# Optimization experiments

Measured on AMD Instinct MI355X. Metric: run time of the kernel, lower is better.

## Reference

```python
import jax, jax.numpy as jnp
import numpy as np

B, T = 128, 256
H = 200                      # hidden_dim
EMB, POSD, NERD = 300, 30, 30
VOCAB, NPOS, NNER = 40000, 50, 25
NCLASS = 2
IN = EMB + POSD + NERD


def setup_inputs():
    key = jax.random.key(0)
    ks = jax.random.split(key, 32)
    words = jax.random.randint(ks[0], (B, T), 1, VOCAB)
    lengths = jax.random.randint(ks[1], (B,), T // 2, T + 1)
    t = jnp.arange(T)
    masks = (t[None, :] >= lengths[:, None]).astype(jnp.int64)  # 1 = pad
    pos = jax.random.randint(ks[2], (B, T), 0, NPOS)
    ner = jax.random.randint(ks[3], (B, T), 0, NNER)

    def span_pos(k, span):  # relative position encoding, 0 on entity span
        start = jax.random.randint(k, (B,), 0, T // 2 - span)
        rel = t[None, :] - start[:, None]
        return jnp.where(rel < 0, rel, jnp.where(rel < span, 0, rel - span + 1)).astype(jnp.int64)

    subj_pos = span_pos(ks[4], 3)
    obj_pos = span_pos(ks[5], 2)

    s = 0.08
    def rn(k, shape):
        return jax.random.normal(k, shape, dtype=jnp.float32) * s

    p = {}
    p["emb_w"] = rn(ks[6], (VOCAB, EMB)).at[0].set(0.0)  # PAD row
    p["pos_w"] = rn(ks[7], (NPOS, POSD))
    p["ner_w"] = rn(ks[8], (NNER, NERD))
    dims = [IN, 2 * H]
    i = 9
    for l in range(2):
        for d in ("f", "b"):
            p["w_ih_l%d%s" % (l, d)] = rn(ks[i], (4 * H, dims[l])); i += 1
            p["w_hh_l%d%s" % (l, d)] = rn(ks[i], (4 * H, H)); i += 1
            p["b_l%d%s" % (l, d)] = rn(ks[i], (4 * H,)); i += 1
    p["wo_w"] = rn(ks[i], (H, 2 * H)); p["wo_b"] = rn(ks[i + 1], (H,))
    p["ws_w"] = rn(ks[i + 2], (H, 2 * H)); p["ws_b"] = rn(ks[i + 3], (H,))
    p["wg_w"] = rn(ks[i + 4], (H, 2 * H)); p["wg_b"] = rn(ks[i + 5], (H,))
    p["cls_w"] = rn(ks[i + 6], (NCLASS, H)); p["cls_b"] = rn(ks[i + 7], (NCLASS,))
    return dict(words=words, masks=masks, pos=pos, ner=ner,
                subj_pos=subj_pos, obj_pos=obj_pos, **p)


def lstm_dir(x, keep, w_ih, w_hh, b, reverse):
    """Packed-sequence-equivalent LSTM: state frozen and output zeroed at pads.
    x: [B,T,D], keep: [B,T] (1.0 = real token). Returns ([B,T,H], final h [B,H])."""
    Hh = w_hh.shape[1]

    def step(carry, inp):
        h, c = carry
        xt, mt = inp  # [B,D], [B,1]
        g = xt @ w_ih.T + h @ w_hh.T + b
        i, f, gg, o = jnp.split(g, 4, axis=-1)  # torch gate order i,f,g,o
        cn = jax.nn.sigmoid(f) * c + jax.nn.sigmoid(i) * jnp.tanh(gg)
        hn = jax.nn.sigmoid(o) * jnp.tanh(cn)
        h = mt * hn + (1.0 - mt) * h
        c = mt * cn + (1.0 - mt) * c
        return (h, c), h * mt

    b_ = x.shape[0]
    h0 = jnp.zeros((b_, Hh), x.dtype)
    xs = (jnp.swapaxes(x, 0, 1), keep.T[..., None])
    (hT, _), ys = jax.lax.scan(step, (h0, h0), xs, reverse=reverse)
    return jnp.swapaxes(ys, 0, 1), hT


def attn_pool(q, kv, pad):
    # single-query attention: q [B,D], kv [B,T,D], pad [B,T] bool
    d_k = q.shape[-1]
    scores = jnp.einsum("bd,btd->bt", q, kv) / jnp.sqrt(jnp.float32(d_k))
    scores = jnp.where(pad, jnp.float32(-1e9), scores)
    p = jax.nn.softmax(scores, axis=-1)
    return jnp.einsum("bt,btd->bd", p, kv)


def _forward(words, masks, pos, ner, subj_pos, obj_pos,
             emb_w, pos_w, ner_w,
             w_ih_l0f, w_hh_l0f, b_l0f, w_ih_l0b, w_hh_l0b, b_l0b,
             w_ih_l1f, w_hh_l1f, b_l1f, w_ih_l1b, w_hh_l1b, b_l1b,
             wo_w, wo_b, ws_w, ws_b, wg_w, wg_b, cls_w, cls_b):
    embs = jnp.concatenate([emb_w[words], pos_w[pos], ner_w[ner]], axis=-1)
    keep = (masks == 0).astype(embs.dtype)
    of0, _ = lstm_dir(embs, keep, w_ih_l0f, w_hh_l0f, b_l0f, False)
    ob0, _ = lstm_dir(embs, keep, w_ih_l0b, w_hh_l0b, b_l0b, True)
    x1 = jnp.concatenate([of0, ob0], axis=-1)
    of1, hf1 = lstm_dir(x1, keep, w_ih_l1f, w_hh_l1f, b_l1f, False)
    ob1, hb1 = lstm_dir(x1, keep, w_ih_l1b, w_hh_l1b, b_l1b, True)
    rnn_out = jnp.concatenate([of1, ob1], axis=-1)  # [B,T,2H]

    pad = masks != 0
    # masked gather-sum over entity spans: (rel_pos + mask) == 0 selects span tokens
    subj_sel = ((subj_pos + masks) == 0).astype(rnn_out.dtype)[..., None]
    obj_sel = ((obj_pos + masks) == 0).astype(rnn_out.dtype)[..., None]
    subj_h = jnp.sum(rnn_out * subj_sel, axis=1)  # [B,2H]
    obj_h = jnp.sum(rnn_out * obj_sel, axis=1)
    glob_h = jnp.concatenate([hb1, hf1], axis=-1)  # hidden[-1]=last bwd, hidden[-2]=last fwd

    obj_a = attn_pool(obj_h, rnn_out, pad)
    subj_a = attn_pool(subj_h, rnn_out, pad)
    glob_a = attn_pool(glob_h, rnn_out, pad)

    h = jax.nn.relu(obj_a @ wo_w.T + wo_b + subj_a @ ws_w.T + ws_b + glob_a @ wg_w.T + wg_b)
    return h @ cls_w.T + cls_b  # [B, NCLASS]


def reference(words, masks, pos, ner, subj_pos, obj_pos,
              emb_w, pos_w, ner_w,
              w_ih_l0f, w_hh_l0f, b_l0f, w_ih_l0b, w_hh_l0b, b_l0b,
              w_ih_l1f, w_hh_l1f, b_l1f, w_ih_l1b, w_hh_l1b, b_l1b,
              wo_w, wo_b, ws_w, ws_b, wg_w, wg_b, cls_w, cls_b):
    return _forward(words, masks, pos, ner, subj_pos, obj_pos,
                    emb_w, pos_w, ner_w,
                    w_ih_l0f, w_hh_l0f, b_l0f, w_ih_l0b, w_hh_l0b, b_l0b,
                    w_ih_l1f, w_hh_l1f, b_l1f, w_ih_l1b, w_hh_l1b, b_l1b,
                    wo_w, wo_b, ws_w, ws_b, wg_w, wg_b, cls_w, cls_b)
```

## Files before the change

kernel.cpp:

```cpp
#include <hip/hip_runtime.h>
#include <hip/hip_bf16.h>
#include <math.h>

constexpr int B = 128;
constexpr int T = 256;
constexpr int H = 200;
constexpr int G4 = 800;
constexpr int BT = B * T;
constexpr int K0 = 360, K0P = 384;
constexpr int K1 = 400, K1P = 416;

typedef __bf16 bf16x8 __attribute__((ext_vector_type(8)));
typedef float f32x4 __attribute__((ext_vector_type(4)));
typedef _Float16 half2v __attribute__((ext_vector_type(2)));
typedef unsigned uix4 __attribute__((ext_vector_type(4)));

__device__ __forceinline__ float bfr2f(unsigned short u) {
  union { unsigned int i; float f; } x;
  x.i = ((unsigned int)u) << 16;
  return x.f;
}
__device__ __forceinline__ unsigned short f2hu(float f) {
  _Float16 h = (_Float16)f;
  return *(unsigned short*)&h;
}
__device__ __forceinline__ half2v ash2(unsigned u) {
  union { unsigned v; half2v h; } x;
  x.v = u;
  return x.h;
}
__device__ __forceinline__ float sigm(float x) {
  return 1.0f / (1.0f + __expf(-x));
}
__device__ __forceinline__ float tanh_f(float x) {
  float e = __expf(2.0f * x);
  return (e - 1.0f) / (e + 1.0f);
}
__device__ __forceinline__ float ldraw(const void* p, size_t i, int f) {
  return f ? ((const float*)p)[i] : bfr2f(((const unsigned short*)p)[i]);
}

__global__ void detect_dtype(const unsigned short* __restrict__ raw,
                             int* __restrict__ flag) {
  __shared__ int cnt[256];
  int c = 0;
  for (int j = 0; j < 32; ++j) {
    unsigned short u = raw[1024 + threadIdx.x * 32 + j];
    int e = (u >> 7) & 0xFF;
    if (e >= 0xC0) ++c;
  }
  cnt[threadIdx.x] = c;
  __syncthreads();
  for (int off = 128; off > 0; off >>= 1) {
    if (threadIdx.x < off) cnt[threadIdx.x] += cnt[threadIdx.x + off];
    __syncthreads();
  }
  if (threadIdx.x == 0) *flag = (cnt[0] > 16) ? 1 : 0;
}

__global__ void fill_zero(uix4* __restrict__ p, size_t n4) {
  size_t i = (size_t)blockIdx.x * blockDim.x + threadIdx.x;
  size_t stride = (size_t)gridDim.x * blockDim.x;
  uix4 z = {0u, 0u, 0u, 0u};
  for (; i < n4; i += stride) p[i] = z;
}

__global__ void embed_kernel(const int* __restrict__ words,
                             const int* __restrict__ pos,
                             const int* __restrict__ ner,
                             const void* __restrict__ emb_w,
                             const void* __restrict__ pos_w,
                             const void* __restrict__ ner_w,
                             __hip_bfloat16* __restrict__ X0,
                             const int* __restrict__ flag) {
  int bt = blockIdx.x;
  int f = *flag;
  int w = words[bt], p = pos[bt], nr = ner[bt];
  for (int j = threadIdx.x; j < K0P; j += blockDim.x) {
    float v;
    if (j < 300)       v = ldraw(emb_w, (size_t)w * 300 + j, f);
    else if (j < 330)  v = ldraw(pos_w, (size_t)p * 30 + (j - 300), f);
    else if (j < 360)  v = ldraw(ner_w, (size_t)nr * 30 + (j - 330), f);
    else               v = 0.0f;
    X0[(size_t)bt * K0P + j] = __float2bfloat16(v);
  }
}

__global__ void pad_copy2(const void* __restrict__ srcf,
                          const void* __restrict__ srcb,
                          __hip_bfloat16* __restrict__ dst, int K, int Kp,
                          const int* __restrict__ flag) {
  int r = blockIdx.x;
  int f = *flag;
  const void* src = (r < G4) ? srcf : srcb;
  int rr = (r < G4) ? r : r - G4;
  for (int j = threadIdx.x; j < Kp; j += blockDim.x) {
    float v = (j < K) ? ldraw(src, (size_t)rr * K + j, f) : 0.0f;
    dst[(size_t)r * Kp + j] = __float2bfloat16(v);
  }
}

__global__ void pack_whh4(const void* __restrict__ s0, const void* __restrict__ s1,
                          const void* __restrict__ s2, const void* __restrict__ s3,
                          unsigned* __restrict__ dst,
                          const int* __restrict__ flag) {
  int idx = blockIdx.x * blockDim.x + threadIdx.x;
  if (idx >= 4 * G4 * 100) return;
  int f = *flag;
  int m = idx / (G4 * 100);
  int loc = idx - m * (G4 * 100);
  const void* src = (m == 0) ? s0 : (m == 1) ? s1 : (m == 2) ? s2 : s3;
  int n = loc / 100, p = loc - n * 100;
  float lo_f = ldraw(src, (size_t)n * 200 + 2 * p, f);
  float hi_f = ldraw(src, (size_t)n * 200 + 2 * p + 1, f);
  dst[idx] = (unsigned)f2hu(lo_f) | ((unsigned)f2hu(hi_f) << 16);
}

__global__ __launch_bounds__(256) void gemm_bt(
    const __hip_bfloat16* __restrict__ A,
    const __hip_bfloat16* __restrict__ Bm,
    __hip_bfloat16* __restrict__ C,
    int N, int Kp) {
  const int lane = threadIdx.x & 63;
  const int wave = threadIdx.x >> 6;
  const int l15 = lane & 15, quad = lane >> 4;
  const int m0 = blockIdx.x * 64 + (wave & 1) * 32;
  const int n0 = blockIdx.y * 128 + (wave >> 1) * 64;

  f32x4 acc[2][4] = {};

  size_t br[4];
  #pragma unroll
  for (int j = 0; j < 4; ++j) {
    int c = n0 + 16 * j + l15;
    if (c > N - 1) c = N - 1;
    br[j] = (size_t)c * Kp;
  }
  const size_t ar0 = (size_t)(m0 + l15) * Kp;
  const size_t ar1 = (size_t)(m0 + 16 + l15) * Kp;

  for (int k0 = 0; k0 < Kp; k0 += 32) {
    int ko = k0 + quad * 8;
    bf16x8 a0 = *(const bf16x8*)(A + ar0 + ko);
    bf16x8 a1 = *(const bf16x8*)(A + ar1 + ko);
    #pragma unroll
    for (int j = 0; j < 4; ++j) {
      bf16x8 b = *(const bf16x8*)(Bm + br[j] + ko);
      acc[0][j] = __builtin_amdgcn_mfma_f32_16x16x32_bf16(a0, b, acc[0][j], 0, 0, 0);
      acc[1][j] = __builtin_amdgcn_mfma_f32_16x16x32_bf16(a1, b, acc[1][j], 0, 0, 0);
    }
  }
  #pragma unroll
  for (int mi = 0; mi < 2; ++mi)
    #pragma unroll
    for (int ni = 0; ni < 4; ++ni)
      #pragma unroll
      for (int r = 0; r < 4; ++r) {
        int row = m0 + mi * 16 + quad * 4 + r;
        int col = n0 + ni * 16 + l15;
        if (col < N)
          C[(size_t)row * N + col] = __float2bfloat16(acc[mi][ni][r]);
      }
}

__global__ __launch_bounds__(512, 2) void lstm_row(
    const __hip_bfloat16* __restrict__ Gpre,
    const unsigned* __restrict__ Wpack,
    const void* __restrict__ bias_f_raw,
    const void* __restrict__ bias_b_raw,
    const int* __restrict__ masks,
    __hip_bfloat16* __restrict__ out,
    int ostride,
    float* __restrict__ final_h,
    const int* __restrict__ flag)
{
  const int tid = threadIdx.x;
  const int dir = blockIdx.x >> 7;
  const int row = blockIdx.x & 127;
  const int wave = tid >> 6;
  const int lane = tid & 63;
  const int kq = wave & 3;
  const int gs = ((wave >> 2) << 6) | lane;
  const bool tail = (gs >= 96);

  __shared__ __align__(16) _Float16 hsh[256];
  __shared__ float parts[4 * 804];
  __shared__ int lensh[256];
  __shared__ int bigbuf[21504];

  const unsigned* wb = Wpack + (size_t)dir * G4 * 100;

  for (int i = tid; i < 3200; i += 512) {
    int g = i / 100, c = i - g * 100;
    bigbuf[g * 101 + c] = (int)wb[(768 + g) * 100 + c];
  }
  if (tid < 256) lensh[tid] = (masks[row * T + tid] == 0) ? 1 : 0;

  unsigned w[6][25];
  {
    const unsigned* s = wb + gs * 100 + kq * 25;
    #pragma unroll
    for (int j = 0; j < 6; ++j)
      #pragma unroll
      for (int p = 0; p < 25; ++p)
        w[j][p] = s[12800 * j + p];
  }
  const unsigned* wt = (const unsigned*)&bigbuf[(gs - 96) * 101 + kq * 25];

  const int u = tid;
  const int f = *flag;
  const void* braw = dir ? bias_b_raw : bias_f_raw;
  float bI = 0.f, bF = 0.f, bG = 0.f, bO = 0.f;
  if (u < 200) {
    bI = ldraw(braw, u, f);
    bF = ldraw(braw, 200 + u, f);
    bG = ldraw(braw, 400 + u, f);
    bO = ldraw(braw, 600 + u, f);
  }

  if (tid < 256) hsh[tid] = (_Float16)0.0f;
  float creg = 0.0f, hreg = 0.0f;
  __syncthreads();

  for (int off = 128; off > 0; off >>= 1) {
    if (tid < off) lensh[tid] += lensh[tid + off];
    __syncthreads();
  }
  const int len = lensh[0];

  const unsigned short* gp = (const unsigned short*)Gpre + dir * 800;
  const size_t gbase = (size_t)row * T;
  const uix4* hvp = (const uix4*)((const char*)hsh + kq * 128);
  const int hwrite = (u / 50) * 64 + (u % 50);

  #pragma unroll 1
  for (int tt = 0; tt < len; ++tt) {
    const int t = dir ? (len - 1 - tt) : tt;
    const size_t goff = (gbase + t) * 1600;
    unsigned short qI = 0, qF = 0, qG = 0, qO = 0;
    if (u < 200) {
      qI = gp[goff + u];
      qF = gp[goff + 200 + u];
      qG = gp[goff + 400 + u];
      qO = gp[goff + 600 + u];
    }

    uix4 hb[7];
    #pragma unroll
    for (int i = 0; i < 7; ++i) hb[i] = hvp[i];

    float a0 = 0.f, a1 = 0.f, a2 = 0.f, a3 = 0.f, a4 = 0.f, a5 = 0.f;
    #pragma unroll
    for (int p = 0; p < 25; ++p) {
      half2v h2 = ash2(hb[p >> 2][p & 3]);
      a0 = __builtin_amdgcn_fdot2(ash2(w[0][p]), h2, a0, false);
      a1 = __builtin_amdgcn_fdot2(ash2(w[1][p]), h2, a1, false);
      a2 = __builtin_amdgcn_fdot2(ash2(w[2][p]), h2, a2, false);
      a3 = __builtin_amdgcn_fdot2(ash2(w[3][p]), h2, a3, false);
      a4 = __builtin_amdgcn_fdot2(ash2(w[4][p]), h2, a4, false);
      a5 = __builtin_amdgcn_fdot2(ash2(w[5][p]), h2, a5, false);
    }
    const int pb = kq * 804;
    parts[pb + gs]        = a0;
    parts[pb + 128 + gs]  = a1;
    parts[pb + 256 + gs]  = a2;
    parts[pb + 384 + gs]  = a3;
    parts[pb + 512 + gs]  = a4;
    parts[pb + 640 + gs]  = a5;
    if (tail) {
      float a6 = 0.f;
      #pragma unroll
      for (int p = 0; p < 25; ++p)
        a6 = __builtin_amdgcn_fdot2(ash2(wt[p]), ash2(hb[p >> 2][p & 3]), a6, false);
      parts[pb + 672 + gs] = a6;
    }
    __syncthreads();

    if (u < 200) {
      float gi = parts[u]       + parts[804 + u]       + parts[1608 + u]       + parts[2412 + u]       + bI + bfr2f(qI);
      float gf = parts[200 + u] + parts[804 + 200 + u] + parts[1608 + 200 + u] + parts[2412 + 200 + u] + bF + bfr2f(qF);
      float gg = parts[400 + u] + parts[804 + 400 + u] + parts[1608 + 400 + u] + parts[2412 + 400 + u] + bG + bfr2f(qG);
      float go = parts[600 + u] + parts[804 + 600 + u] + parts[1608 + 600 + u] + parts[2412 + 600 + u] + bO + bfr2f(qO);
      float si = sigm(gi), sf = sigm(gf), so = sigm(go);
      float cn = sf * creg + si * tanh_f(gg);
      float hn = so * tanh_f(cn);
      creg = cn;
      hreg = hn;
      hsh[hwrite] = (_Float16)hn;
      out[((size_t)row * T + t) * ostride + dir * H + u] = __float2bfloat16(hn);
    }
    __syncthreads();
  }

  if (final_h != nullptr && u < 200) {
    int col = dir ? u : (H + u);
    final_h[(size_t)row * 400 + col] = hreg;
  }
}

__global__ __launch_bounds__(256) void span_sum(
    const __hip_bfloat16* __restrict__ rnn,
    const int* __restrict__ masks,
    const int* __restrict__ subj_pos,
    const int* __restrict__ obj_pos,
    float* __restrict__ obj_h,
    float* __restrict__ subj_h)
{
  int b = blockIdx.x;
  int tc = threadIdx.x >> 6;
  int dv = threadIdx.x & 63;
  __shared__ float aS[4][400];
  __shared__ float aO[4][400];

  float ss[8] = {}, so[8] = {};
  if (dv < 50) {
    for (int t = tc * 64; t < tc * 64 + 64; ++t) {
      int m = masks[b * T + t];
      int fs = (subj_pos[b * T + t] + m) == 0;
      int fo = (obj_pos[b * T + t] + m) == 0;
      if (fs | fo) {
        uix4 v = *(const uix4*)(rnn + ((size_t)b * T + t) * 400 + dv * 8);
        #pragma unroll
        for (int j = 0; j < 4; ++j) {
          float lo = bfr2f((unsigned short)(v[j] & 0xFFFF));
          float hi = bfr2f((unsigned short)(v[j] >> 16));
          if (fs) { ss[2 * j] += lo; ss[2 * j + 1] += hi; }
          if (fo) { so[2 * j] += lo; so[2 * j + 1] += hi; }
        }
      }
    }
    #pragma unroll
    for (int k = 0; k < 8; ++k) {
      aS[tc][dv * 8 + k] = ss[k];
      aO[tc][dv * 8 + k] = so[k];
    }
  }
  __syncthreads();
  for (int d = threadIdx.x; d < 400; d += 256) {
    subj_h[(size_t)b * 400 + d] = aS[0][d] + aS[1][d] + aS[2][d] + aS[3][d];
    obj_h[(size_t)b * 400 + d]  = aO[0][d] + aO[1][d] + aO[2][d] + aO[3][d];
  }
}

__global__ __launch_bounds__(256) void attn_pool_k(
    const float* __restrict__ qbuf,
    const __hip_bfloat16* __restrict__ rnn,
    const int* __restrict__ masks,
    float* __restrict__ outp)
{
  int b = blockIdx.x & 127;
  int qi = blockIdx.x >> 7;
  __shared__ float qs[400];
  __shared__ float ps[256];
  __shared__ float red[256];
  __shared__ float acc4[4][400];
  const float* q = qbuf + ((size_t)qi * B + b) * 400;
  for (int d = threadIdx.x; d < 400; d += 256) qs[d] = q[d];
  __syncthreads();

  int t = threadIdx.x;
  const uix4* kvv = (const uix4*)(rnn + ((size_t)b * T + t) * 400);
  float s = 0.f;
  #pragma unroll 5
  for (int i = 0; i < 50; ++i) {
    uix4 v = kvv[i];
    #pragma unroll
    for (int j = 0; j < 4; ++j) {
      s += bfr2f((unsigned short)(v[j] & 0xFFFF)) * qs[8 * i + 2 * j];
      s += bfr2f((unsigned short)(v[j] >> 16))    * qs[8 * i + 2 * j + 1];
    }
  }
  s *= 0.05f;
  if (masks[b * T + t] != 0) s = -1e9f;

  red[t] = s;
  __syncthreads();
  for (int off = 128; off > 0; off >>= 1) {
    if (t < off) red[t] = fmaxf(red[t], red[t + off]);
    __syncthreads();
  }
  float mx = red[0];
  __syncthreads();
  float e = expf(s - mx);
  red[t] = e;
  __syncthreads();
  for (int off = 128; off > 0; off >>= 1) {
    if (t < off) red[t] += red[t + off];
    __syncthreads();
  }
  float inv = 1.0f / red[0];
  ps[t] = e * inv;
  __syncthreads();

  int tc = threadIdx.x >> 6;
  int dv = threadIdx.x & 63;
  float a[8] = {};
  if (dv < 50) {
    for (int t2 = tc * 64; t2 < tc * 64 + 64; ++t2) {
      float wgt = ps[t2];
      if (wgt != 0.f) {
        uix4 v = *(const uix4*)(rnn + ((size_t)b * T + t2) * 400 + dv * 8);
        #pragma unroll
        for (int j = 0; j < 4; ++j) {
          a[2 * j]     += wgt * bfr2f((unsigned short)(v[j] & 0xFFFF));
          a[2 * j + 1] += wgt * bfr2f((unsigned short)(v[j] >> 16));
        }
      }
    }
    #pragma unroll
    for (int k = 0; k < 8; ++k) acc4[tc][dv * 8 + k] = a[k];
  }
  __syncthreads();
  for (int d = threadIdx.x; d < 400; d += 256)
    outp[((size_t)qi * B + b) * 400 + d] =
        acc4[0][d] + acc4[1][d] + acc4[2][d] + acc4[3][d];
}

__global__ __launch_bounds__(256) void final_head(
    const float* __restrict__ attn,
    const void* __restrict__ wo_w, const void* __restrict__ wo_b,
    const void* __restrict__ ws_w, const void* __restrict__ ws_b,
    const void* __restrict__ wg_w, const void* __restrict__ wg_b,
    const void* __restrict__ cls_w, const void* __restrict__ cls_b,
    void* __restrict__ outp,
    const int* __restrict__ flag)
{
  int b = blockIdx.x;
  int f = *flag;
  __shared__ float hs[H];
  int j = threadIdx.x;
  if (j < H) {
    float acc = ldraw(wo_b, j, f) + ldraw(ws_b, j, f) + ldraw(wg_b, j, f);
    const float* oa = attn + ((size_t)0 * B + b) * 400;
    const float* sa = attn + ((size_t)1 * B + b) * 400;
    const float* ga = attn + ((size_t)2 * B + b) * 400;
    for (int d = 0; d < 400; ++d) {
      acc += oa[d] * ldraw(wo_w, (size_t)j * 400 + d, f);
      acc += sa[d] * ldraw(ws_w, (size_t)j * 400 + d, f);
      acc += ga[d] * ldraw(wg_w, (size_t)j * 400 + d, f);
    }
    hs[j] = fmaxf(acc, 0.0f);
  }
  __syncthreads();
  if (j < 2) {
    float a = ldraw(cls_b, j, f);
    for (int k = 0; k < H; ++k)
      a += hs[k] * ldraw(cls_w, (size_t)j * H + k, f);
    if (f) ((float*)outp)[b * 2 + j] = a;
    else   ((__hip_bfloat16*)outp)[b * 2 + j] = __float2bfloat16(a);
  }
}

constexpr size_t O_X0   = 0;
constexpr size_t O_X1   = 25165824;
constexpr size_t O_GPRE = 52428800;
constexpr size_t O_RNN  = 157286400;
constexpr size_t O_WIH0 = 183500800;
constexpr size_t O_WIH1 = 184729600;
constexpr size_t O_WPK  = 186060800;
constexpr size_t O_Q    = 187340800;
constexpr size_t O_ATT  = 187955200;
constexpr size_t O_FLAG = 188569600;

extern "C" void kernel_launch(void* const* d_in, const int* in_sizes, int n_in,
                              void* d_out, int out_size, void* d_ws, size_t ws_size,
                              hipStream_t stream) {
  (void)in_sizes; (void)n_in; (void)out_size; (void)ws_size;

  const int* words = (const int*)d_in[0];
  const int* masks = (const int*)d_in[1];
  const int* pos   = (const int*)d_in[2];
  const int* ner   = (const int*)d_in[3];
  const int* subj  = (const int*)d_in[4];
  const int* obj   = (const int*)d_in[5];
  const void* emb_w = d_in[6];
  const void* pos_w = d_in[7];
  const void* ner_w = d_in[8];
  const void* wih[4]  = {d_in[9],  d_in[12], d_in[15], d_in[18]};
  const void* whh[4]  = {d_in[10], d_in[13], d_in[16], d_in[19]};
  const void* bias[4] = {d_in[11], d_in[14], d_in[17], d_in[20]};
  const void* wo_w = d_in[21]; const void* wo_b = d_in[22];
  const void* ws_w = d_in[23]; const void* ws_b = d_in[24];
  const void* wg_w = d_in[25]; const void* wg_b = d_in[26];
  const void* cls_w = d_in[27]; const void* cls_b = d_in[28];

  char* ws = (char*)d_ws;
  __hip_bfloat16* X0   = (__hip_bfloat16*)(ws + O_X0);
  __hip_bfloat16* X1   = (__hip_bfloat16*)(ws + O_X1);
  __hip_bfloat16* Gpre = (__hip_bfloat16*)(ws + O_GPRE);
  __hip_bfloat16* RNN  = (__hip_bfloat16*)(ws + O_RNN);
  __hip_bfloat16* wih0p = (__hip_bfloat16*)(ws + O_WIH0);
  __hip_bfloat16* wih1p = (__hip_bfloat16*)(ws + O_WIH1);
  unsigned* Wpack = (unsigned*)(ws + O_WPK);
  float* qbuf = (float*)(ws + O_Q);
  float* attb = (float*)(ws + O_ATT);
  int* flag = (int*)(ws + O_FLAG);

  detect_dtype<<<1, 256, 0, stream>>>((const unsigned short*)emb_w, flag);
  pack_whh4<<<1250, 256, 0, stream>>>(whh[0], whh[1], whh[2], whh[3], Wpack, flag);
  pad_copy2<<<1600, 128, 0, stream>>>(wih[0], wih[1], wih0p, K0, K0P, flag);
  pad_copy2<<<1600, 128, 0, stream>>>(wih[2], wih[3], wih1p, K1, K1P, flag);

  embed_kernel<<<BT, 128, 0, stream>>>(words, pos, ner, emb_w, pos_w, ner_w, X0, flag);
  fill_zero<<<1024, 256, 0, stream>>>((uix4*)X1, (size_t)BT * K1P * 2 / 16);
  fill_zero<<<1024, 256, 0, stream>>>((uix4*)RNN, (size_t)BT * 400 * 2 / 16);

  dim3 ggrid(BT / 64, 13);

  gemm_bt<<<ggrid, 256, 0, stream>>>(X0, wih0p, Gpre, 1600, K0P);
  lstm_row<<<256, 512, 0, stream>>>(Gpre, Wpack, bias[0], bias[1], masks,
                                    X1, K1P, nullptr, flag);

  gemm_bt<<<ggrid, 256, 0, stream>>>(X1, wih1p, Gpre, 1600, K1P);
  float* qglob = qbuf + (size_t)2 * B * 400;
  lstm_row<<<256, 512, 0, stream>>>(Gpre, Wpack + (size_t)2 * G4 * 100,
                                    bias[2], bias[3], masks,
                                    RNN, 400, qglob, flag);

  span_sum<<<B, 256, 0, stream>>>(RNN, masks, subj, obj,
                                  qbuf, qbuf + (size_t)B * 400);

  attn_pool_k<<<3 * B, 256, 0, stream>>>(qbuf, RNN, masks, attb);

  final_head<<<B, 256, 0, stream>>>(attb, wo_w, wo_b, ws_w, ws_b, wg_w, wg_b,
                                    cls_w, cls_b, d_out, flag);
}
```

Before: 1.385 ms.

## Tile input-projection GEMM through double-buffered swizzled LDS with 128x128 blocks

Rewrites the input-to-hidden GEMM so each block stages 128x64 tiles of A and B into shared memory with an XOR swizzle. Global loads for the next K tile are issued into registers while MFMAs run on the current buffer. Each wave now computes a 64x64 output tile instead of 32x64, and the grid is halved in M to match. The goal is to cut redundant global loads and raise MFMA reuse, at the cost of more registers and LDS per block, which may lower occupancy. Tail K tiles are zero-filled when the padded K is not a multiple of 64.

New measurement: 1.153 ms. 16.7% less time.

```diff
diff --git a/kernel.cpp b/kernel.cpp
--- a/kernel.cpp
+++ b/kernel.cpp
@@ -121,43 +121,95 @@
     const __hip_bfloat16* __restrict__ Bm,
     __hip_bfloat16* __restrict__ C,
     int N, int Kp) {
-  const int lane = threadIdx.x & 63;
-  const int wave = threadIdx.x >> 6;
+  const int tid = threadIdx.x;
+  const int lane = tid & 63;
+  const int wave = tid >> 6;
   const int l15 = lane & 15, quad = lane >> 4;
-  const int m0 = blockIdx.x * 64 + (wave & 1) * 32;
-  const int n0 = blockIdx.y * 128 + (wave >> 1) * 64;
-
-  f32x4 acc[2][4] = {};
-
-  size_t br[4];
+  const int wr = wave & 1, wc = wave >> 1;
+  const int m0 = blockIdx.x * 128;
+  const int n0 = blockIdx.y * 128;
+
+  __shared__ __align__(16) __hip_bfloat16 Ab[2][128 * 64];
+  __shared__ __align__(16) __hip_bfloat16 Bb[2][128 * 64];
+
+  f32x4 acc[4][4] = {};
+
+  const int nk = (Kp + 63) >> 6;
+
+  uix4 st[8];
+  auto stage_issue = [&](int kt) {
+    const int k0 = kt << 6;
+    #pragma unroll
+    for (int j = 0; j < 8; ++j) {
+      int c = tid + (j & 3) * 256;
+      int row = c >> 3, p = c & 7;
+      int qd = p ^ (row & 7);
+      int kcol = k0 + qd * 8;
+      uix4 z = {0u, 0u, 0u, 0u};
+      if (kcol + 8 <= Kp) {
+        if (j < 4) {
+          st[j] = *(const uix4*)(A + (size_t)(m0 + row) * Kp + kcol);
+        } else {
+          int br = n0 + row; if (br > N - 1) br = N - 1;
+          st[j] = *(const uix4*)(Bm + (size_t)br * Kp + kcol);
+        }
+      } else {
+        st[j] = z;
+      }
+    }
+  };
+  auto stage_write = [&](int buf) {
+    #pragma unroll
+    for (int j = 0; j < 8; ++j) {
+      int c = tid + (j & 3) * 256;
+      if (j < 4) *(uix4*)((char*)&Ab[buf][0] + c * 16) = st[j];
+      else       *(uix4*)((char*)&Bb[buf][0] + c * 16) = st[j];
+    }
+  };
+
+  stage_issue(0);
+  stage_write(0);
+  __syncthreads();
+
+  for (int kt = 0; kt < nk; ++kt) {
+    const int buf = kt & 1;
+    if (kt + 1 < nk) stage_issue(kt + 1);
+
+    #pragma unroll
+    for (int k32 = 0; k32 < 2; ++k32) {
+      bf16x8 a[4], b[4];
+      #pragma unroll
+      for (int mi = 0; mi < 4; ++mi) {
+        int row = wr * 64 + mi * 16 + l15;
+        int p = (k32 * 4 + quad) ^ (row & 7);
+        a[mi] = *(const bf16x8*)((const char*)&Ab[buf][0] + (row * 8 + p) * 16);
+      }
+      #pragma unroll
+      for (int ni = 0; ni < 4; ++ni) {
+        int row = wc * 64 + ni * 16 + l15;
+        int p = (k32 * 4 + quad) ^ (row & 7);
+        b[ni] = *(const bf16x8*)((const char*)&Bb[buf][0] + (row * 8 + p) * 16);
+      }
+      #pragma unroll
+      for (int mi = 0; mi < 4; ++mi)
+        #pragma unroll
+        for (int ni = 0; ni < 4; ++ni)
+          acc[mi][ni] = __builtin_amdgcn_mfma_f32_16x16x32_bf16(
+              a[mi], b[ni], acc[mi][ni], 0, 0, 0);
+    }
+
+    if (kt + 1 < nk) stage_write((kt + 1) & 1);
+    __syncthreads();
+  }
+
   #pragma unroll
-  for (int j = 0; j < 4; ++j) {
-    int c = n0 + 16 * j + l15;
-    if (c > N - 1) c = N - 1;
-    br[j] = (size_t)c * Kp;
-  }
-  const size_t ar0 = (size_t)(m0 + l15) * Kp;
-  const size_t ar1 = (size_t)(m0 + 16 + l15) * Kp;
-
-  for (int k0 = 0; k0 < Kp; k0 += 32) {
-    int ko = k0 + quad * 8;
-    bf16x8 a0 = *(const bf16x8*)(A + ar0 + ko);
-    bf16x8 a1 = *(const bf16x8*)(A + ar1 + ko);
-    #pragma unroll
-    for (int j = 0; j < 4; ++j) {
-      bf16x8 b = *(const bf16x8*)(Bm + br[j] + ko);
-      acc[0][j] = __builtin_amdgcn_mfma_f32_16x16x32_bf16(a0, b, acc[0][j], 0, 0, 0);
-      acc[1][j] = __builtin_amdgcn_mfma_f32_16x16x32_bf16(a1, b, acc[1][j], 0, 0, 0);
-    }
-  }
-  #pragma unroll
-  for (int mi = 0; mi < 2; ++mi)
+  for (int mi = 0; mi < 4; ++mi)
     #pragma unroll
     for (int ni = 0; ni < 4; ++ni)
       #pragma unroll
       for (int r = 0; r < 4; ++r) {
-        int row = m0 + mi * 16 + quad * 4 + r;
-        int col = n0 + ni * 16 + l15;
+        int row = m0 + wr * 64 + mi * 16 + quad * 4 + r;
+        int col = n0 + wc * 64 + ni * 16 + l15;
         if (col < N)
           C[(size_t)row * N + col] = __float2bfloat16(acc[mi][ni][r]);
       }
@@ -505,7 +557,7 @@
   fill_zero<<<1024, 256, 0, stream>>>((uix4*)X1, (size_t)BT * K1P * 2 / 16);
   fill_zero<<<1024, 256, 0, stream>>>((uix4*)RNN, (size_t)BT * 400 * 2 / 16);
 
-  dim3 ggrid(BT / 64, 13);
+  dim3 ggrid(BT / 128, 13);
 
   gemm_bt<<<ggrid, 256, 0, stream>>>(X0, wih0p, Gpre, 1600, K0P);
   lstm_row<<<256, 512, 0, stream>>>(Gpre, Wpack, bias[0], bias[1], masks,
```
